# Kernel optimization log

Hardware: AMD Instinct MI355X
Metric: run time of the kernel (lower is better)

Reference implementation:

```python
import jax, jax.numpy as jnp
import numpy as np

N_NODES = 50000
N_EDGES = 600000
IN_DIM = 128
HID_DIM = 128
OUT_DIM = 128
N_GRAPHS = 64


def _glorot(key, shape):
    lim = np.sqrt(6.0 / (shape[0] + shape[1]))
    return jax.random.uniform(key, shape, jnp.float32, -lim, lim)


def setup_inputs() -> dict:
    key = jax.random.key(0)
    ks = jax.random.split(key, 8)
    h = jax.random.normal(ks[0], (N_NODES, IN_DIM), jnp.float32)
    src = jax.random.randint(ks[1], (N_EDGES,), 0, N_NODES, jnp.int64)
    dst = jax.random.randint(ks[2], (N_EDGES,), 0, N_NODES, jnp.int64)
    graph_ids = jnp.sort(jax.random.randint(ks[3], (N_NODES,), 0, N_GRAPHS, jnp.int64))
    W1 = _glorot(ks[4], (IN_DIM, HID_DIM)); b1 = jnp.zeros((HID_DIM,), jnp.float32)
    W2 = _glorot(ks[5], (HID_DIM, HID_DIM)); b2 = jnp.zeros((HID_DIM,), jnp.float32)
    W3 = _glorot(ks[6], (HID_DIM, OUT_DIM)); b3 = jnp.zeros((OUT_DIM,), jnp.float32)
    return {"h": h, "src": src, "dst": dst, "graph_ids": graph_ids,
            "W1": W1, "b1": b1, "W2": W2, "b2": b2, "W3": W3, "b3": b3,
            "n_graphs": N_GRAPHS}


def _graph_conv(h, src, dst, norm_src, norm_dst, W, b):
    # DGL GraphConv, norm='both': D_dst^{-1/2} A^T D_src^{-1/2} h W + b
    m = h * norm_src[:, None]                                   # [N, d]
    agg = jax.ops.segment_sum(m[src], dst, num_segments=h.shape[0])  # [N, d]
    return (agg * norm_dst[:, None]) @ W + b


def reference(h, src, dst, graph_ids, W1, b1, W2, b2, W3, b3, n_graphs):
    n = h.shape[0]
    ones = jnp.ones((src.shape[0],), h.dtype)
    out_deg = jnp.clip(jax.ops.segment_sum(ones, src, num_segments=n), 1.0)
    in_deg = jnp.clip(jax.ops.segment_sum(ones, dst, num_segments=n), 1.0)
    norm_src = out_deg ** -0.5
    norm_dst = in_deg ** -0.5

    x = jax.nn.relu(_graph_conv(h, src, dst, norm_src, norm_dst, W1, b1))
    x = jax.nn.relu(_graph_conv(x, src, dst, norm_src, norm_dst, W2, b2))
    x = jax.nn.relu(_graph_conv(x, src, dst, norm_src, norm_dst, W3, b3))

    # dgl.mean_nodes: per-graph mean over nodes
    gsum = jax.ops.segment_sum(x, graph_ids, num_segments=n_graphs)          # [G, d]
    gcnt = jax.ops.segment_sum(jnp.ones((n,), x.dtype), graph_ids, num_segments=n_graphs)
    return gsum / jnp.clip(gcnt, 1.0)[:, None]
```

## Files before the change

### kernel.cpp

```cpp
#include <hip/hip_runtime.h>
#include <hip/hip_fp16.h>


#define DIM 128
#define GRAPHS 64

typedef _Float16 half8 __attribute__((ext_vector_type(8)));
typedef _Float16 half4 __attribute__((ext_vector_type(4)));
typedef float floatx4 __attribute__((ext_vector_type(4)));

#define HIST_R 4
#define HIST_S 64
#define NPR 12500
#define LDSW (NPR / 2)

__global__ __launch_bounds__(256) void k_hist(const int* __restrict__ src,
                                              const int* __restrict__ dst,
                                              unsigned* __restrict__ partial, int E) {
    __shared__ __align__(16) unsigned hist[LDSW];
    int b = blockIdx.x;
    int a = b / (HIST_R * HIST_S);
    int r = (b / HIST_S) % HIST_R;
    int s = b % HIST_S;
    const int* arr = a ? dst : src;
    for (int i = threadIdx.x; i < LDSW; i += 256) hist[i] = 0;
    __syncthreads();
    int chunk = (E + HIST_S - 1) / HIST_S;
    int e0 = s * chunk;
    int e1 = min(e0 + chunk, E);
    unsigned base = (unsigned)(r * NPR);
    for (int i = e0 + threadIdx.x; i < e1; i += 256) {
        unsigned n = (unsigned)arr[i] - base;
        if (n < NPR) atomicAdd(&hist[n >> 1], 1u << ((n & 1) * 16));
    }
    __syncthreads();
    uint2* outp = (uint2*)(partial + ((size_t)(a * HIST_R + r) * HIST_S + s) * LDSW);
    const uint2* h2 = (const uint2*)hist;
    for (int i = threadIdx.x; i < LDSW / 2; i += 256) outp[i] = h2[i];
}

__global__ __launch_bounds__(256) void k_hist_merge(const unsigned* __restrict__ partial,
                                                    float* __restrict__ ns,
                                                    float* __restrict__ nd,
                                                    int* __restrict__ inc,
                                                    int* __restrict__ bsum, int N) {
    __shared__ int sred[256];
    int nb = (N + 255) / 256;
    int isDst = (blockIdx.x < nb) ? 1 : 0;
    int cb = isDst ? blockIdx.x : blockIdx.x - nb;
    int n = cb * 256 + threadIdx.x;
    int deg = 0;
    if (n < N) {
        int a = isDst ? 1 : 0;
        int r = n / NPR;
        int w = (n % NPR) >> 1;
        int field = (n & 1) * 16;
        const unsigned* p = partial + ((size_t)(a * HIST_R + r) * HIST_S) * LDSW + w;
        unsigned sum = 0;
#pragma unroll
        for (int s = 0; s < HIST_S; ++s) sum += p[(size_t)s * LDSW];
        deg = (int)((sum >> field) & 0xFFFFu);
        float nrm = rsqrtf(fmaxf((float)deg, 1.0f));
        if (isDst) { nd[n] = nrm; inc[n] = deg; }
        else       { ns[n] = nrm; }
    }
    if (isDst) {
        sred[threadIdx.x] = deg;
        __syncthreads();
        for (int off = 128; off > 0; off >>= 1) {
            if (threadIdx.x < off) sred[threadIdx.x] += sred[threadIdx.x + off];
            __syncthreads();
        }
        if (threadIdx.x == 0) bsum[cb] = sred[0];
    }
}

__global__ __launch_bounds__(256) void k_scan_prep(
    const int* __restrict__ inc, const int* __restrict__ bsum,
    const unsigned* __restrict__ partial, int* __restrict__ row_ptr,
    int* __restrict__ cur, float* __restrict__ gsum,
    const float4* __restrict__ h, const float* __restrict__ ns,
    uint2* __restrict__ A, const float* __restrict__ W1,
    const float* __restrict__ W2, const float* __restrict__ W3,
    _Float16* __restrict__ Wt1, _Float16* __restrict__ Wt2,
    _Float16* __restrict__ Wt3, int N) {
    __shared__ int sb[256];
    __shared__ int s[256];
    __shared__ int exs[256];
    int nb = (N + 255) / 256;
    int t = threadIdx.x;

    if (blockIdx.x >= nb) {
        int i = (blockIdx.x - nb) * 256 + t;
        int nf4 = N * 32;
        if (i < nf4) {
            int n = i >> 5;
            float sc = ns[n];
            float4 v = h[i];
            __half2 p0 = __floats2half2_rn(v.x * sc, v.y * sc);
            __half2 p1 = __floats2half2_rn(v.z * sc, v.w * sc);
            uint2 o;
            o.x = *(unsigned*)&p0;
            o.y = *(unsigned*)&p1;
            A[i] = o;
        } else {
            int j = i - nf4;
            if (j < 3 * 16384) {
                int which = j >> 14;
                int local = j & 16383;
                int k = local >> 7;
                int n = local & 127;
                const float* W = (which == 0) ? W1 : (which == 1) ? W2 : W3;
                _Float16* Wt = (which == 0) ? Wt1 : (which == 1) ? Wt2 : Wt3;
                Wt[(size_t)n * DIM + k] = (_Float16)W[local];
            }
        }
        return;
    }

    int bv = (t < nb) ? bsum[t] : 0;
    sb[t] = bv;
    __syncthreads();
    for (int off = 1; off < 256; off <<= 1) {
        int u = (t >= off) ? sb[t - off] : 0;
        __syncthreads();
        sb[t] += u;
        __syncthreads();
    }
    int excl = sb[t] - bv;
    __syncthreads();
    sb[t] = excl;
    __syncthreads();
    int blockBase = sb[blockIdx.x];

    int B = blockIdx.x * 256;
    int i = B + t;
    int v = (i < N) ? inc[i] : 0;
    s[t] = v;
    __syncthreads();
    for (int off = 1; off < 256; off <<= 1) {
        int u = (t >= off) ? s[t - off] : 0;
        __syncthreads();
        s[t] += u;
        __syncthreads();
    }
    int ex = blockBase + s[t] - v;
    exs[t] = ex;
    if (i < N) row_ptr[i] = ex;
    if (i == N - 1) row_ptr[N] = ex + v;
    if (blockIdx.x == 0) {
        for (int j = t; j < GRAPHS * DIM; j += 256) gsum[j] = 0.0f;
    }
    __syncthreads();

    if (t < 128) {
        int n0 = B + 2 * t;
        if (n0 < N) {
            int r = n0 / NPR;
            int w = (n0 % NPR) >> 1;
            const unsigned* p = partial + ((size_t)(HIST_R + r) * HIST_S) * LDSW + w;
            int run0 = exs[2 * t];
            int run1 = exs[2 * t + 1];
            int* c = cur + (size_t)r * HIST_S * NPR + 2 * w;
#pragma unroll
            for (int sl = 0; sl < HIST_S; ++sl) {
                c[(size_t)sl * NPR + 0] = run0;
                c[(size_t)sl * NPR + 1] = run1;
                unsigned hv = p[(size_t)sl * LDSW];
                run0 += (int)(hv & 0xFFFFu);
                run1 += (int)(hv >> 16);
            }
        }
    }
}

__global__ __launch_bounds__(256) void k_fill2(const int* __restrict__ src,
                                               const int* __restrict__ dst,
                                               const int* __restrict__ cur,
                                               int* __restrict__ csr, int E) {
    __shared__ __align__(16) int lcur[NPR];
    int r = blockIdx.x / HIST_S;
    int s = blockIdx.x % HIST_S;
    const int4* cs4 = (const int4*)(cur + (size_t)(r * HIST_S + s) * NPR);
    int4* l4 = (int4*)lcur;
    for (int i = threadIdx.x; i < NPR / 4; i += 256) l4[i] = cs4[i];
    __syncthreads();
    int chunk = (E + HIST_S - 1) / HIST_S;
    int e0 = s * chunk;
    int e1 = min(e0 + chunk, E);
    unsigned base = (unsigned)(r * NPR);
    for (int i = e0 + threadIdx.x; i < e1; i += 256) {
        unsigned d = (unsigned)dst[i] - base;
        if (d < NPR) {
            int p = atomicAdd(&lcur[d], 1);
            csr[p] = src[i];
        }
    }
}

__global__ __launch_bounds__(256) void k_agg(const uint4* __restrict__ A,
                                             const int* __restrict__ row_ptr,
                                             const int* __restrict__ csr,
                                             const float* __restrict__ nd,
                                             uint4* __restrict__ Bh, int N) {
    int gtid = blockIdx.x * blockDim.x + threadIdx.x;
    int node = gtid >> 6;
    int lane = threadIdx.x & 63;
    if (node >= N) return;
    int e0 = row_ptr[node];
    int e1 = row_ptr[node + 1];
    int grp = lane >> 4;
    int l16 = lane & 15;
    float acc[8];
#pragma unroll
    for (int k = 0; k < 8; ++k) acc[k] = 0.0f;

    for (int base = e0; base < e1; base += 32) {
        int vl = csr[min(base + (lane & 31), e1 - 1)];
        uint4 u[8];
#pragma unroll
        for (int j = 0; j < 8; ++j) {
            int idx = __shfl(vl, 4 * j + grp);
            u[j] = A[(size_t)idx * 16 + l16];
        }
#pragma unroll
        for (int j = 0; j < 8; ++j) {
            if (base + 4 * j + grp < e1) {
                __half2 h0 = *(__half2*)&u[j].x;
                __half2 h1 = *(__half2*)&u[j].y;
                __half2 h2 = *(__half2*)&u[j].z;
                __half2 h3 = *(__half2*)&u[j].w;
                float2 f0 = __half22float2(h0);
                float2 f1 = __half22float2(h1);
                float2 f2 = __half22float2(h2);
                float2 f3 = __half22float2(h3);
                acc[0] += f0.x; acc[1] += f0.y;
                acc[2] += f1.x; acc[3] += f1.y;
                acc[4] += f2.x; acc[5] += f2.y;
                acc[6] += f3.x; acc[7] += f3.y;
            }
        }
    }

#pragma unroll
    for (int k = 0; k < 8; ++k) {
        float v = acc[k];
        v += __shfl_xor(v, 16);
        v += __shfl_xor(v, 32);
        acc[k] = v;
    }

    if (grp == 0) {
        float s = nd[node];
        __half2 p0 = __floats2half2_rn(acc[0] * s, acc[1] * s);
        __half2 p1 = __floats2half2_rn(acc[2] * s, acc[3] * s);
        __half2 p2 = __floats2half2_rn(acc[4] * s, acc[5] * s);
        __half2 p3 = __floats2half2_rn(acc[6] * s, acc[7] * s);
        uint4 o;
        o.x = *(unsigned*)&p0;
        o.y = *(unsigned*)&p1;
        o.z = *(unsigned*)&p2;
        o.w = *(unsigned*)&p3;
        Bh[(size_t)node * 16 + l16] = o;
    }
}

template <bool SCALE_NS>
__global__ __launch_bounds__(256) void k_gemm_t(
    const _Float16* __restrict__ Bin, const _Float16* __restrict__ Wt,
    const float* __restrict__ bias, const float* __restrict__ ns,
    _Float16* __restrict__ Xout, int N) {
    int tid = threadIdx.x;
    int wave = tid >> 6;
    int lane = tid & 63;
    int quad = lane >> 4;
    int l16 = lane & 15;
    int node = blockIdx.x * 64 + wave * 16 + l16;

    half8 b[4];
#pragma unroll
    for (int q = 0; q < 4; ++q) {
        if (node < N) {
            b[q] = *(const half8*)&Bin[(size_t)node * DIM + q * 32 + quad * 8];
        } else {
            b[q] = half8{0, 0, 0, 0, 0, 0, 0, 0};
        }
    }

    floatx4 acc[8];
#pragma unroll
    for (int c = 0; c < 8; ++c) acc[c] = floatx4{0.f, 0.f, 0.f, 0.f};

#pragma unroll
    for (int c = 0; c < 8; ++c) {
#pragma unroll
        for (int q = 0; q < 4; ++q) {
            half8 a = *(const half8*)&Wt[(size_t)(c * 16 + l16) * DIM + q * 32 + quad * 8];
            acc[c] = __builtin_amdgcn_mfma_f32_16x16x32_f16(a, b[q], acc[c], 0, 0, 0);
        }
    }

    if (node < N) {
        float s = SCALE_NS ? ns[node] : 1.0f;
#pragma unroll
        for (int c = 0; c < 8; ++c) {
            float4 b4 = *(const float4*)&bias[c * 16 + quad * 4];
            half4 o;
            o[0] = (_Float16)(fmaxf(acc[c][0] + b4.x, 0.0f) * s);
            o[1] = (_Float16)(fmaxf(acc[c][1] + b4.y, 0.0f) * s);
            o[2] = (_Float16)(fmaxf(acc[c][2] + b4.z, 0.0f) * s);
            o[3] = (_Float16)(fmaxf(acc[c][3] + b4.w, 0.0f) * s);
            *(half4*)&Xout[(size_t)node * DIM + c * 16 + quad * 4] = o;
        }
    }
}

#define PBINS 8
__global__ __launch_bounds__(256) void k_gemm_pool(
    const _Float16* __restrict__ Bin, const _Float16* __restrict__ Wt,
    const float* __restrict__ bias, const int* __restrict__ gid,
    float* __restrict__ gsum, int N) {
    __shared__ float lsum[PBINS * DIM];
    int tid = threadIdx.x;
    for (int i = tid; i < PBINS * DIM; i += 256) lsum[i] = 0.0f;
    int wave = tid >> 6;
    int lane = tid & 63;
    int quad = lane >> 4;
    int l16 = lane & 15;
    int r0 = blockIdx.x * 64;
    int node = r0 + wave * 16 + l16;
    int nodec = min(node, N - 1);

    half8 b[4];
#pragma unroll
    for (int q = 0; q < 4; ++q) {
        if (node < N) {
            b[q] = *(const half8*)&Bin[(size_t)node * DIM + q * 32 + quad * 8];
        } else {
            b[q] = half8{0, 0, 0, 0, 0, 0, 0, 0};
        }
    }

    floatx4 acc[8];
#pragma unroll
    for (int c = 0; c < 8; ++c) acc[c] = floatx4{0.f, 0.f, 0.f, 0.f};
    __syncthreads();

#pragma unroll
    for (int c = 0; c < 8; ++c) {
#pragma unroll
        for (int q = 0; q < 4; ++q) {
            half8 a = *(const half8*)&Wt[(size_t)(c * 16 + l16) * DIM + q * 32 + quad * 8];
            acc[c] = __builtin_amdgcn_mfma_f32_16x16x32_f16(a, b[q], acc[c], 0, 0, 0);
        }
    }

    int g = gid[nodec];
    int g0b = gid[r0];
    int gEb = gid[min(r0 + 63, N - 1)];
    bool ldsPath = (gEb - g0b) < PBINS;
    int gF = __shfl(g, 0);
    int gL = __shfl(g, 15);
    bool uni = (gF == gL);
    float valid = (node < N) ? 1.0f : 0.0f;

#pragma unroll
    for (int c = 0; c < 8; ++c) {
        float4 b4 = *(const float4*)&bias[c * 16 + quad * 4];
        float bv[4] = {b4.x, b4.y, b4.z, b4.w};
#pragma unroll
        for (int r = 0; r < 4; ++r) {
            float v = fmaxf(acc[c][r] + bv[r], 0.0f) * valid;
            int f = c * 16 + quad * 4 + r;
            if (ldsPath) {
                if (uni) {
                    v += __shfl_xor(v, 1);
                    v += __shfl_xor(v, 2);
                    v += __shfl_xor(v, 4);
                    v += __shfl_xor(v, 8);
                    if (l16 == 0) atomicAdd(&lsum[(gF - g0b) * DIM + f], v);
                } else {
                    if (node < N) atomicAdd(&lsum[(g - g0b) * DIM + f], v);
                }
            } else {
                if (node < N) atomicAdd(&gsum[(size_t)g * DIM + f], v);
            }
        }
    }
    __syncthreads();
    if (ldsPath) {
        int ng = gEb - g0b + 1;
        for (int i = tid; i < ng * DIM; i += 256) {
            float sv = lsum[i];
            if (sv != 0.0f) atomicAdd(&gsum[(size_t)g0b * DIM + i], sv);
        }
    }
}

__global__ void k_finalize(const float* __restrict__ gsum, const int* __restrict__ gid,
                           float* __restrict__ out, int N, int G) {
    int i = blockIdx.x * blockDim.x + threadIdx.x;
    if (i < G * DIM) {
        int g = i >> 7;
        int lo = 0, hi = N;
        while (lo < hi) { int m = (lo + hi) >> 1; if (gid[m] < g) lo = m + 1; else hi = m; }
        int lo2 = lo, hi2 = N;
        while (lo2 < hi2) { int m = (lo2 + hi2) >> 1; if (gid[m] < g + 1) lo2 = m + 1; else hi2 = m; }
        float c = fmaxf((float)(lo2 - lo), 1.0f);
        out[i] = gsum[i] / c;
    }
}

extern "C" void kernel_launch(void* const* d_in, const int* in_sizes, int n_in,
                              void* d_out, int out_size, void* d_ws, size_t ws_size,
                              hipStream_t stream) {
    const float* h   = (const float*)d_in[0];
    const int*   src = (const int*)d_in[1];
    const int*   dst = (const int*)d_in[2];
    const int*   gid = (const int*)d_in[3];
    const float* W1  = (const float*)d_in[4];
    const float* b1  = (const float*)d_in[5];
    const float* W2  = (const float*)d_in[6];
    const float* b2  = (const float*)d_in[7];
    const float* W3  = (const float*)d_in[8];
    const float* b3  = (const float*)d_in[9];

    const int N = in_sizes[0] / DIM;
    const int E = in_sizes[1];
    const int G = GRAPHS;
    float* out = (float*)d_out;

    char* ws = (char*)d_ws;
    size_t off = 0;
    auto alloc = [&](size_t bytes) -> void* {
        void* p = ws + off;
        off += (bytes + 255) & ~(size_t)255;
        return p;
    };
    const int nb = (N + 255) / 256;
    uint2* Ah0     = (uint2*)alloc((size_t)N * DIM * 2);
    uint2* Ah1     = (uint2*)alloc((size_t)N * DIM * 2);
    uint2* Bh      = (uint2*)alloc((size_t)N * DIM * 2);
    _Float16* Wt1  = (_Float16*)alloc((size_t)DIM * DIM * 2);
    _Float16* Wt2  = (_Float16*)alloc((size_t)DIM * DIM * 2);
    _Float16* Wt3  = (_Float16*)alloc((size_t)DIM * DIM * 2);
    float* ns      = (float*)alloc((size_t)N * 4);
    float* nd      = (float*)alloc((size_t)N * 4);
    int*   inc     = (int*)alloc((size_t)N * 4);
    unsigned* partial = (unsigned*)alloc((size_t)2 * HIST_R * HIST_S * LDSW * 4);
    int*   cur     = (int*)alloc((size_t)HIST_R * HIST_S * NPR * 4);
    int*   row_ptr = (int*)alloc((size_t)(N + 1) * 4);
    int*   csr     = (int*)alloc((size_t)E * 4);
    float* gsum    = (float*)alloc((size_t)G * DIM * 4);
    int*   bsum    = (int*)alloc((size_t)nb * 4);

    k_hist<<<2 * HIST_R * HIST_S, 256, 0, stream>>>(src, dst, partial, E);
    k_hist_merge<<<2 * nb, 256, 0, stream>>>(partial, ns, nd, inc, bsum, N);
    int prepBlocks = (N * 32 + 3 * 16384 + 255) / 256;
    k_scan_prep<<<nb + prepBlocks, 256, 0, stream>>>(inc, bsum, partial, row_ptr, cur,
                                                     gsum, (const float4*)h, ns, Ah0,
                                                     W1, W2, W3, Wt1, Wt2, Wt3, N);
    k_fill2<<<HIST_R * HIST_S, 256, 0, stream>>>(src, dst, cur, csr, E);

    int aggBlocks  = (N * 64 + 255) / 256;
    int gemmBlocks = (N + 63) / 64;

    k_agg<<<aggBlocks, 256, 0, stream>>>((const uint4*)Ah0, row_ptr, csr, nd, (uint4*)Bh, N);
    k_gemm_t<true><<<gemmBlocks, 256, 0, stream>>>((const _Float16*)Bh, Wt1, b1, ns, (_Float16*)Ah1, N);
    k_agg<<<aggBlocks, 256, 0, stream>>>((const uint4*)Ah1, row_ptr, csr, nd, (uint4*)Bh, N);
    k_gemm_t<true><<<gemmBlocks, 256, 0, stream>>>((const _Float16*)Bh, Wt2, b2, ns, (_Float16*)Ah0, N);
    k_agg<<<aggBlocks, 256, 0, stream>>>((const uint4*)Ah0, row_ptr, csr, nd, (uint4*)Bh, N);
    k_gemm_pool<<<gemmBlocks, 256, 0, stream>>>((const _Float16*)Bh, Wt3, b3, gid, gsum, N);

    k_finalize<<<(G * DIM + 255) / 256, 256, 0, stream>>>(gsum, gid, out, N, G);
}
```

Baseline: 306.1 us.

## Halve histogram node ranges and fold finalize into pool via last-block counter

The degree histogram now splits nodes into 2 ranges of 25000 instead of 4 ranges of 12500. This halves the number of histogram blocks and the times each block rescans the edge arrays, at the cost of a larger LDS histogram per block. The fill kernel keeps its 4-range layout, and the scan now maps between the two partitions. The separate finalize kernel is removed: the last pool block, found through an atomic counter with a threadfence, divides the sums by the graph counts. This saves a launch but adds a serial tail in one block.

```diff
diff --git a/kernel.cpp b/kernel.cpp
--- a/kernel.cpp
+++ b/kernel.cpp
@@ -9,34 +9,36 @@
 typedef _Float16 half4 __attribute__((ext_vector_type(4)));
 typedef float floatx4 __attribute__((ext_vector_type(4)));
 
-#define HIST_R 4
+#define HR2 2
+#define NP2 25000
+#define LW2 (NP2 / 2)
 #define HIST_S 64
+#define FILL_R 4
 #define NPR 12500
-#define LDSW (NPR / 2)
 
 __global__ __launch_bounds__(256) void k_hist(const int* __restrict__ src,
                                               const int* __restrict__ dst,
                                               unsigned* __restrict__ partial, int E) {
-    __shared__ __align__(16) unsigned hist[LDSW];
+    __shared__ __align__(16) unsigned hist[LW2];
     int b = blockIdx.x;
-    int a = b / (HIST_R * HIST_S);
-    int r = (b / HIST_S) % HIST_R;
+    int a = b / (HR2 * HIST_S);
+    int r = (b / HIST_S) % HR2;
     int s = b % HIST_S;
     const int* arr = a ? dst : src;
-    for (int i = threadIdx.x; i < LDSW; i += 256) hist[i] = 0;
+    for (int i = threadIdx.x; i < LW2; i += 256) hist[i] = 0;
     __syncthreads();
     int chunk = (E + HIST_S - 1) / HIST_S;
     int e0 = s * chunk;
     int e1 = min(e0 + chunk, E);
-    unsigned base = (unsigned)(r * NPR);
+    unsigned base = (unsigned)(r * NP2);
     for (int i = e0 + threadIdx.x; i < e1; i += 256) {
         unsigned n = (unsigned)arr[i] - base;
-        if (n < NPR) atomicAdd(&hist[n >> 1], 1u << ((n & 1) * 16));
-    }
-    __syncthreads();
-    uint2* outp = (uint2*)(partial + ((size_t)(a * HIST_R + r) * HIST_S + s) * LDSW);
+        if (n < NP2) atomicAdd(&hist[n >> 1], 1u << ((n & 1) * 16));
+    }
+    __syncthreads();
+    uint2* outp = (uint2*)(partial + ((size_t)(a * HR2 + r) * HIST_S + s) * LW2);
     const uint2* h2 = (const uint2*)hist;
-    for (int i = threadIdx.x; i < LDSW / 2; i += 256) outp[i] = h2[i];
+    for (int i = threadIdx.x; i < LW2 / 2; i += 256) outp[i] = h2[i];
 }
 
 __global__ __launch_bounds__(256) void k_hist_merge(const unsigned* __restrict__ partial,
@@ -52,13 +54,13 @@
     int deg = 0;
     if (n < N) {
         int a = isDst ? 1 : 0;
-        int r = n / NPR;
-        int w = (n % NPR) >> 1;
+        int r = n / NP2;
+        int w = (n % NP2) >> 1;
         int field = (n & 1) * 16;
-        const unsigned* p = partial + ((size_t)(a * HIST_R + r) * HIST_S) * LDSW + w;
+        const unsigned* p = partial + ((size_t)(a * HR2 + r) * HIST_S) * LW2 + w;
         unsigned sum = 0;
 #pragma unroll
-        for (int s = 0; s < HIST_S; ++s) sum += p[(size_t)s * LDSW];
+        for (int s = 0; s < HIST_S; ++s) sum += p[(size_t)s * LW2];
         deg = (int)((sum >> field) & 0xFFFFu);
         float nrm = rsqrtf(fmaxf((float)deg, 1.0f));
         if (isDst) { nd[n] = nrm; inc[n] = deg; }
@@ -78,7 +80,7 @@
 __global__ __launch_bounds__(256) void k_scan_prep(
     const int* __restrict__ inc, const int* __restrict__ bsum,
     const unsigned* __restrict__ partial, int* __restrict__ row_ptr,
-    int* __restrict__ cur, float* __restrict__ gsum,
+    int* __restrict__ cur, float* __restrict__ gsum, int* __restrict__ done,
     const float4* __restrict__ h, const float* __restrict__ ns,
     uint2* __restrict__ A, const float* __restrict__ W1,
     const float* __restrict__ W2, const float* __restrict__ W3,
@@ -150,23 +152,26 @@
     if (i == N - 1) row_ptr[N] = ex + v;
     if (blockIdx.x == 0) {
         for (int j = t; j < GRAPHS * DIM; j += 256) gsum[j] = 0.0f;
+        if (t == 0) done[0] = 0;
     }
     __syncthreads();
 
     if (t < 128) {
         int n0 = B + 2 * t;
         if (n0 < N) {
-            int r = n0 / NPR;
-            int w = (n0 % NPR) >> 1;
-            const unsigned* p = partial + ((size_t)(HIST_R + r) * HIST_S) * LDSW + w;
+            int r2 = n0 / NP2;
+            int w2 = (n0 % NP2) >> 1;
+            const unsigned* p = partial + ((size_t)(HR2 + r2) * HIST_S) * LW2 + w2;
+            int r4 = n0 / NPR;
+            int wf = (n0 % NPR) >> 1;
             int run0 = exs[2 * t];
             int run1 = exs[2 * t + 1];
-            int* c = cur + (size_t)r * HIST_S * NPR + 2 * w;
+            int* c = cur + (size_t)r4 * HIST_S * NPR + 2 * wf;
 #pragma unroll
             for (int sl = 0; sl < HIST_S; ++sl) {
                 c[(size_t)sl * NPR + 0] = run0;
                 c[(size_t)sl * NPR + 1] = run1;
-                unsigned hv = p[(size_t)sl * LDSW];
+                unsigned hv = p[(size_t)sl * LW2];
                 run0 += (int)(hv & 0xFFFFu);
                 run1 += (int)(hv >> 16);
             }
@@ -319,8 +324,10 @@
 __global__ __launch_bounds__(256) void k_gemm_pool(
     const _Float16* __restrict__ Bin, const _Float16* __restrict__ Wt,
     const float* __restrict__ bias, const int* __restrict__ gid,
-    float* __restrict__ gsum, int N) {
+    float* __restrict__ gsum, int* __restrict__ done,
+    float* __restrict__ out, int N) {
     __shared__ float lsum[PBINS * DIM];
+    __shared__ int lastFlag;
     int tid = threadIdx.x;
     for (int i = tid; i < PBINS * DIM; i += 256) lsum[i] = 0.0f;
     int wave = tid >> 6;
@@ -395,19 +402,22 @@
             if (sv != 0.0f) atomicAdd(&gsum[(size_t)g0b * DIM + i], sv);
         }
     }
-}
-
-__global__ void k_finalize(const float* __restrict__ gsum, const int* __restrict__ gid,
-                           float* __restrict__ out, int N, int G) {
-    int i = blockIdx.x * blockDim.x + threadIdx.x;
-    if (i < G * DIM) {
-        int g = i >> 7;
-        int lo = 0, hi = N;
-        while (lo < hi) { int m = (lo + hi) >> 1; if (gid[m] < g) lo = m + 1; else hi = m; }
-        int lo2 = lo, hi2 = N;
-        while (lo2 < hi2) { int m = (lo2 + hi2) >> 1; if (gid[m] < g + 1) lo2 = m + 1; else hi2 = m; }
-        float c = fmaxf((float)(lo2 - lo), 1.0f);
-        out[i] = gsum[i] / c;
+
+    __threadfence();
+    __syncthreads();
+    if (tid == 0) lastFlag = (atomicAdd(done, 1) == (int)gridDim.x - 1) ? 1 : 0;
+    __syncthreads();
+    if (lastFlag) {
+        __threadfence();
+        for (int i = tid; i < GRAPHS * DIM; i += 256) {
+            int gg = i >> 7;
+            int lo = 0, hi = N;
+            while (lo < hi) { int m = (lo + hi) >> 1; if (gid[m] < gg) lo = m + 1; else hi = m; }
+            int lo2 = lo, hi2 = N;
+            while (lo2 < hi2) { int m = (lo2 + hi2) >> 1; if (gid[m] < gg + 1) lo2 = m + 1; else hi2 = m; }
+            float c = fmaxf((float)(lo2 - lo), 1.0f);
+            out[i] = gsum[i] / c;
+        }
     }
 }
 
@@ -429,6 +439,7 @@
     const int E = in_sizes[1];
     const int G = GRAPHS;
     float* out = (float*)d_out;
+    (void)G;
 
     char* ws = (char*)d_ws;
     size_t off = 0;
@@ -447,20 +458,21 @@
     float* ns      = (float*)alloc((size_t)N * 4);
     float* nd      = (float*)alloc((size_t)N * 4);
     int*   inc     = (int*)alloc((size_t)N * 4);
-    unsigned* partial = (unsigned*)alloc((size_t)2 * HIST_R * HIST_S * LDSW * 4);
-    int*   cur     = (int*)alloc((size_t)HIST_R * HIST_S * NPR * 4);
+    unsigned* partial = (unsigned*)alloc((size_t)2 * HR2 * HIST_S * LW2 * 4);
+    int*   cur     = (int*)alloc((size_t)FILL_R * HIST_S * NPR * 4);
     int*   row_ptr = (int*)alloc((size_t)(N + 1) * 4);
     int*   csr     = (int*)alloc((size_t)E * 4);
-    float* gsum    = (float*)alloc((size_t)G * DIM * 4);
+    float* gsum    = (float*)alloc((size_t)GRAPHS * DIM * 4);
     int*   bsum    = (int*)alloc((size_t)nb * 4);
-
-    k_hist<<<2 * HIST_R * HIST_S, 256, 0, stream>>>(src, dst, partial, E);
+    int*   done    = (int*)alloc(256);
+
+    k_hist<<<2 * HR2 * HIST_S, 256, 0, stream>>>(src, dst, partial, E);
     k_hist_merge<<<2 * nb, 256, 0, stream>>>(partial, ns, nd, inc, bsum, N);
     int prepBlocks = (N * 32 + 3 * 16384 + 255) / 256;
     k_scan_prep<<<nb + prepBlocks, 256, 0, stream>>>(inc, bsum, partial, row_ptr, cur,
-                                                     gsum, (const float4*)h, ns, Ah0,
-                                                     W1, W2, W3, Wt1, Wt2, Wt3, N);
-    k_fill2<<<HIST_R * HIST_S, 256, 0, stream>>>(src, dst, cur, csr, E);
+                                                     gsum, done, (const float4*)h, ns,
+                                                     Ah0, W1, W2, W3, Wt1, Wt2, Wt3, N);
+    k_fill2<<<FILL_R * HIST_S, 256, 0, stream>>>(src, dst, cur, csr, E);
 
     int aggBlocks  = (N * 64 + 255) / 256;
     int gemmBlocks = (N + 63) / 64;
@@ -470,7 +482,6 @@
     k_agg<<<aggBlocks, 256, 0, stream>>>((const uint4*)Ah1, row_ptr, csr, nd, (uint4*)Bh, N);
     k_gemm_t<true><<<gemmBlocks, 256, 0, stream>>>((const _Float16*)Bh, Wt2, b2, ns, (_Float16*)Ah0, N);
     k_agg<<<aggBlocks, 256, 0, stream>>>((const uint4*)Ah0, row_ptr, csr, nd, (uint4*)Bh, N);
-    k_gemm_pool<<<gemmBlocks, 256, 0, stream>>>((const _Float16*)Bh, Wt3, b3, gid, gsum, N);
-
-    k_finalize<<<(G * DIM + 255) / 256, 256, 0, stream>>>(gsum, gid, out, N, G);
-}
+    k_gemm_pool<<<gemmBlocks, 256, 0, stream>>>((const _Float16*)Bh, Wt3, b3, gid, gsum,
+                                                done, out, N);
+}
```

New measurement: 502.0 us. 1.64x slower.
